# Kernel optimization log

Measured on AMD Instinct MI355X. Metric: run time of the kernel, lower is better.

## Reference

```python
import jax, jax.numpy as jnp
import numpy as np

EMBED, HEADS, LEVELS, POINTS = 256, 8, 4, 4
HD = EMBED // HEADS
BS, NQ = 2, 16384
SHAPES = [(128, 128), (64, 64), (32, 32), (16, 16)]  # (H, W) per level
NV = sum(h * w for h, w in SHAPES)
EPS = 1e-5


def layernorm(x, g, b):
    mu = jnp.mean(x, -1, keepdims=True)
    var = jnp.mean((x - mu) ** 2, -1, keepdims=True)
    return (x - mu) / jnp.sqrt(var + EPS) * g + b


def bilinear_sample(vl, loc, H, W):
    # vl: (bs, heads, H*W, hd); loc: (bs, nq, heads, P, 2) normalized [0,1]
    # grid_sample semantics: align_corners=False, zero padding
    x = loc[..., 0] * W - 0.5
    y = loc[..., 1] * H - 0.5
    x0 = jnp.floor(x)
    y0 = jnp.floor(y)
    lx, ly = x - x0, y - y0
    x0 = x0.astype(jnp.int32)
    y0 = y0.astype(jnp.int32)
    gather = jax.vmap(jax.vmap(lambda t, i: t[i]))  # over (bs, heads)
    acc = None
    for dx, dy, w in ((0, 0, (1 - lx) * (1 - ly)), (1, 0, lx * (1 - ly)),
                      (0, 1, (1 - lx) * ly), (1, 1, lx * ly)):
        xi, yi = x0 + dx, y0 + dy
        valid = ((xi >= 0) & (xi < W) & (yi >= 0) & (yi < H)).astype(vl.dtype)
        idx = jnp.clip(yi, 0, H - 1) * W + jnp.clip(xi, 0, W - 1)
        idx = idx.transpose(0, 2, 1, 3)           # (bs, heads, nq, P)
        g = gather(vl, idx)                       # (bs, heads, nq, P, hd)
        wv = (w * valid).transpose(0, 2, 1, 3)[..., None]
        acc = g * wv if acc is None else acc + g * wv
    return acc


def forward(lidar_feat, feat_flatten, ref_2d, spatial_shapes, level_start_index,
            q_pose, W_off, b_off, W_attn, b_attn, W_val, b_val, W_out, b_out,
            ln1_g, ln1_b, ffn_w1, ffn_w2, ln2_g, ln2_b):
    identity = lidar_feat                         # (nq, bs, C)
    q = (lidar_feat + q_pose).transpose(1, 0, 2)  # (bs, nq, C)
    bs, nq, C = q.shape
    v = feat_flatten.transpose(1, 0, 2) @ W_val + b_val
    v = v.reshape(bs, -1, HEADS, HD)
    off = (q @ W_off + b_off).reshape(bs, nq, HEADS, LEVELS, POINTS, 2)
    aw = (q @ W_attn + b_attn).reshape(bs, nq, HEADS, LEVELS * POINTS)
    aw = jax.nn.softmax(aw, -1).reshape(bs, nq, HEADS, LEVELS, POINTS)
    ss = np.asarray(spatial_shapes)               # static level shapes
    lsi = np.asarray(level_start_index)
    norm = jnp.asarray(ss[:, ::-1].copy(), q.dtype)  # (L, 2) [W, H]
    loc = ref_2d[:, :, None, :, None, :] + off / norm[None, None, None, :, None, :]
    out = jnp.zeros((bs, nq, HEADS, HD), q.dtype)
    for l in range(LEVELS):
        H, W = int(ss[l, 0]), int(ss[l, 1])
        s = int(lsi[l])
        vl = v[:, s:s + H * W].transpose(0, 2, 1, 3)   # (bs, heads, HW, hd)
        sampled = bilinear_sample(vl, loc[:, :, :, l], H, W)
        out = out + jnp.einsum('bhqpd,bqhp->bqhd', sampled, aw[:, :, :, l, :])
    out = out.reshape(bs, nq, C) @ W_out + b_out
    out = out.transpose(1, 0, 2) + identity       # residual (dropout=eval noop)
    x = layernorm(out, ln1_g, ln1_b)
    x = layernorm(jnp.maximum(x @ ffn_w1, 0.0) @ ffn_w2 + x, ln2_g, ln2_b)
    return x


def setup_inputs():
    key = jax.random.key(0)
    ks = jax.random.split(key, 16)
    starts = np.cumsum([0] + [h * w for h, w in SHAPES])[:-1]
    d = {
        'lidar_feat': jax.random.normal(ks[0], (NQ, BS, EMBED), jnp.float32),
        'feat_flatten': jax.random.normal(ks[1], (NV, BS, EMBED), jnp.float32),
        'ref_2d': jax.random.uniform(ks[2], (BS, NQ, LEVELS, 2), jnp.float32),
        'spatial_shapes': jnp.array(SHAPES, jnp.int32),
        'level_start_index': jnp.array(starts, jnp.int32),
        'q_pose': jax.random.normal(ks[3], (NQ, BS, EMBED), jnp.float32),
        'W_off': 0.02 * jax.random.normal(ks[4], (EMBED, HEADS * LEVELS * POINTS * 2), jnp.float32),
        'b_off': 2.0 * jax.random.normal(ks[5], (HEADS * LEVELS * POINTS * 2,), jnp.float32),
        'W_attn': 0.02 * jax.random.normal(ks[6], (EMBED, HEADS * LEVELS * POINTS), jnp.float32),
        'b_attn': jnp.zeros((HEADS * LEVELS * POINTS,), jnp.float32),
        'W_val': 0.02 * jax.random.normal(ks[7], (EMBED, EMBED), jnp.float32),
        'b_val': jnp.zeros((EMBED,), jnp.float32),
        'W_out': 0.02 * jax.random.normal(ks[8], (EMBED, EMBED), jnp.float32),
        'b_out': jnp.zeros((EMBED,), jnp.float32),
        'ln1_g': jnp.ones((EMBED,), jnp.float32),
        'ln1_b': jnp.zeros((EMBED,), jnp.float32),
        'ffn_w1': 0.02 * jax.random.normal(ks[9], (EMBED, EMBED), jnp.float32),
        'ffn_w2': 0.02 * jax.random.normal(ks[10], (EMBED, EMBED), jnp.float32),
        'ln2_g': jnp.ones((EMBED,), jnp.float32),
        'ln2_b': jnp.zeros((EMBED,), jnp.float32),
    }
    return d


def reference(lidar_feat, feat_flatten, ref_2d, spatial_shapes, level_start_index,
              q_pose, W_off, b_off, W_attn, b_attn, W_val, b_val, W_out, b_out,
              ln1_g, ln1_b, ffn_w1, ffn_w2, ln2_g, ln2_b):
    return forward(lidar_feat, feat_flatten, ref_2d, spatial_shapes,
                   level_start_index, q_pose, W_off, b_off, W_attn, b_attn,
                   W_val, b_val, W_out, b_out, ln1_g, ln1_b, ffn_w1, ffn_w2,
                   ln2_g, ln2_b)
```

## Files before the change

kernel.cpp:

```cpp
#include <hip/hip_runtime.h>
#include <cstdint>

#define EMBED 256
#define HEADS 8
#define LEVELS 4
#define POINTS 4
#define BS 2
#define NQ 16384
#define NV 21760
#define MQ (BS*NQ)
#define MV (BS*NV)
#define VAL_BLK 340
#define OA_BLK  256
#define BKT_BLK 64

typedef __attribute__((ext_vector_type(8))) short short8;
typedef __attribute__((ext_vector_type(4))) float f32x4;

__device__ __forceinline__ unsigned short f2bf(float f) {
    unsigned int u = __float_as_uint(f);
    u = (u + 0x7FFFu + ((u >> 16) & 1u)) >> 16;
    return (unsigned short)u;
}
__device__ __forceinline__ float bf2f(unsigned short h) {
    return __uint_as_float(((unsigned int)h) << 16);
}
__device__ __forceinline__ void glds16(const unsigned short* g, unsigned short* l) {
    __builtin_amdgcn_global_load_lds((const __attribute__((address_space(1))) void*)g,
                                     (__attribute__((address_space(3))) void*)l, 16, 0, 0);
}

struct WtArgs {
    const float* src[6];
    unsigned short* dst[6];
    int n[6];
};
__global__ __launch_bounds__(256) void prep_wt(WtArgs a, int* __restrict__ hist)
{
    const int t = threadIdx.x;
    if (blockIdx.x == 0 && blockIdx.y == 0) { hist[t] = 0; hist[t + 256] = 0; }
    const int g = blockIdx.y;
    const int N = a.n[g];
    const int e = blockIdx.x * 256 + t;
    if (e >= 256 * N) return;
    const int k = e / N, n = e - k * N;
    a.dst[g][(size_t)n * 256 + k] = f2bf(a.src[g][e]);
}

template<int NCOLS>
__device__ __forceinline__ void gemm_core(
    unsigned short* As, unsigned short* Bs, int bx,
    const float* __restrict__ Af, const float* __restrict__ A2f, int inner,
    const unsigned short* __restrict__ Bt,
    const float* __restrict__ bias0, const float* __restrict__ bias1,
    unsigned short* __restrict__ outh)
{
    constexpr int FN = NCOLS / 64;
    const int t = threadIdx.x, l = t & 63, w = t >> 6;
    const int wm = w >> 2, wn = w & 3;
    const int frow = l & 15, fgrp = l >> 4;
    const size_t brow = (size_t)bx * 128;

    const int fslot = fgrp ^ ((frow & 3) ^ ((frow >> 2) & 3));
    const int srow = l >> 2;
    const int sswz = (l & 3) ^ ((srow & 3) ^ ((srow >> 2) & 3));
    const unsigned short* gB0 = Bt + ((size_t)(w * 16 + srow)) * 256 + sswz * 8;

    const int arow_s = t >> 2, aslot_s = t & 3;
    const int grow = (int)brow + arow_s;
    const int bidx = grow / inner, nn = grow - bidx * inner;
    const float* srcA = Af + (size_t)(nn * BS + bidx) * 256;
    const float* srcA2 = A2f ? A2f + (size_t)(nn * BS + bidx) * 256 : nullptr;
    const int aswz_s = aslot_s ^ ((arow_s & 3) ^ ((arow_s >> 2) & 3));

    f32x4 acc[4][FN];
#pragma unroll
    for (int i = 0; i < 4; ++i)
#pragma unroll
        for (int j = 0; j < FN; ++j) acc[i][j] = f32x4{0.f, 0.f, 0.f, 0.f};

    float4 pA0 = *(const float4*)(srcA + aslot_s * 8);
    float4 pA1 = *(const float4*)(srcA + aslot_s * 8 + 4);
    float4 pC0, pC1;
    if (srcA2) { pC0 = *(const float4*)(srcA2 + aslot_s * 8);
                 pC1 = *(const float4*)(srcA2 + aslot_s * 8 + 4); }

    for (int k0 = 0; k0 < 256; k0 += 32) {
        glds16(gB0 + k0,         &Bs[w * 512]);
        glds16(gB0 + 32768 + k0, &Bs[(w + 8) * 512]);
        if constexpr (NCOLS == 384)
            glds16(gB0 + 65536 + k0, &Bs[(w + 16) * 512]);

        float c[8] = {pA0.x, pA0.y, pA0.z, pA0.w, pA1.x, pA1.y, pA1.z, pA1.w};
        if (srcA2) {
            c[0] += pC0.x; c[1] += pC0.y; c[2] += pC0.z; c[3] += pC0.w;
            c[4] += pC1.x; c[5] += pC1.y; c[6] += pC1.z; c[7] += pC1.w;
        }
        short8 pk;
#pragma unroll
        for (int i = 0; i < 8; ++i) pk[i] = (short)f2bf(c[i]);
        *reinterpret_cast<short8*>(&As[arow_s * 32 + aswz_s * 8]) = pk;
        if (k0 + 32 < 256) {
            pA0 = *(const float4*)(srcA + k0 + 32 + aslot_s * 8);
            pA1 = *(const float4*)(srcA + k0 + 32 + aslot_s * 8 + 4);
            if (srcA2) { pC0 = *(const float4*)(srcA2 + k0 + 32 + aslot_s * 8);
                         pC1 = *(const float4*)(srcA2 + k0 + 32 + aslot_s * 8 + 4); }
        }
        __syncthreads();

        short8 af[4]; short8 bq[FN];
#pragma unroll
        for (int fm = 0; fm < 4; ++fm)
            af[fm] = *reinterpret_cast<const short8*>(&As[(wm * 64 + fm * 16 + frow) * 32 + fslot * 8]);
#pragma unroll
        for (int fn = 0; fn < FN; ++fn)
            bq[fn] = *reinterpret_cast<const short8*>(&Bs[(wn * (NCOLS / 4) + fn * 16 + frow) * 32 + fslot * 8]);
#pragma unroll
        for (int fm = 0; fm < 4; ++fm)
#pragma unroll
            for (int fn = 0; fn < FN; ++fn)
                acc[fm][fn] = __builtin_amdgcn_mfma_f32_16x16x32_bf16(af[fm], bq[fn], acc[fm][fn], 0, 0, 0);
        __syncthreads();
    }

#pragma unroll
    for (int fn = 0; fn < FN; ++fn) {
        const int col = wn * (NCOLS / 4) + fn * 16 + frow;
        float b = 0.f;
        if (NCOLS == 384) b = (col < 256) ? bias0[col] : bias1[col - 256];
        else              b = bias0[col];
#pragma unroll
        for (int fm = 0; fm < 4; ++fm)
#pragma unroll
            for (int j = 0; j < 4; ++j) {
                const size_t row = brow + wm * 64 + fm * 16 + fgrp * 4 + j;
                outh[row * NCOLS + col] = f2bf(acc[fm][fn][j] + b);
            }
    }
}

__global__ __launch_bounds__(512) void valoa_k(
    const float* __restrict__ feat, const float* __restrict__ lidar,
    const float* __restrict__ q_pose, const float* __restrict__ ref2d,
    const unsigned short* __restrict__ wt_val, const unsigned short* __restrict__ wt_oa,
    const float* __restrict__ b_val, const float* __restrict__ b_off,
    const float* __restrict__ b_attn,
    unsigned short* __restrict__ vb, unsigned short* __restrict__ oa,
    int* __restrict__ bkt, int* __restrict__ hist)
{
    __shared__ unsigned short As[128 * 32];
    __shared__ unsigned short Bs[384 * 32];
    const int bx = blockIdx.x;
    if (bx < VAL_BLK) {
        gemm_core<256>(As, Bs, bx, feat, nullptr, NV, wt_val, b_val, nullptr, vb);
    } else if (bx < VAL_BLK + OA_BLK) {
        gemm_core<384>(As, Bs, bx - VAL_BLK, lidar, q_pose, NQ, wt_oa, b_off, b_attn, oa);
    } else {
        const int rb = (bx - VAL_BLK - OA_BLK) * 512 + threadIdx.x;
        const float x = ref2d[(size_t)rb * 8 + 0];
        const float y = ref2d[(size_t)rb * 8 + 1];
        const int qx = min(15, max(0, (int)(x * 16.f)));
        const int qy = min(15, max(0, (int)(y * 16.f)));
        const int bv = (rb >> 14) * 256 + qy * 16 + qx;
        bkt[rb] = bv;
        atomicAdd(&hist[bv], 1);
    }
}

__global__ __launch_bounds__(512) void scan_scatter_k(
    const int* __restrict__ hist, const int* __restrict__ bkt, int* __restrict__ perm)
{
    __shared__ int s[512];
    __shared__ int cur[512];
    const int t = threadIdx.x;
    const int v = hist[t];
    s[t] = v;
    __syncthreads();
    int acc = v;
#pragma unroll
    for (int o = 1; o < 512; o <<= 1) {
        const int add = (t >= o) ? s[t - o] : 0;
        __syncthreads();
        acc += add;
        s[t] = acc;
        __syncthreads();
    }
    cur[t] = acc - v;
    __syncthreads();
#pragma unroll 4
    for (int i = 0; i < 64; ++i) {
        const int rb = i * 512 + t;
        const int pos = atomicAdd(&cur[bkt[rb]], 1);
        perm[pos] = rb;
    }
}

__global__ __launch_bounds__(256) void sampler_k(
    const unsigned short* __restrict__ oa,
    const float* __restrict__ ref2d,
    const unsigned short* __restrict__ v,
    const int* __restrict__ perm,
    unsigned short* __restrict__ outh)
{
    const int bid = blockIdx.x;
    const int sbid = (bid & 7) * (MQ / 4 / 8) + (bid >> 3);
    const int q0 = sbid * 4;
    const int t = threadIdx.x;

    __shared__ uint2 s_d[4][8][4][17];

#pragma unroll
    for (int it = 0; it < 2; ++it) {
        const int item = t + it * 256;
        const int tq = item >> 7, hlp = item & 127;
        const int h = hlp >> 4, lp = hlp & 15, li = lp >> 2;
        const int rb = perm[q0 + tq];
        const int b = rb >> 14;

        const float2 refv = *(const float2*)(ref2d + (size_t)rb * 8 + li * 2);
        const ushort2 offu = *(const ushort2*)(oa + (size_t)rb * 384 + hlp * 2);
        const float ax = bf2f(oa[(size_t)rb * 384 + 256 + hlp]);

        float m = ax;
#pragma unroll
        for (int o = 1; o < 16; o <<= 1) m = fmaxf(m, __shfl_xor(m, o));
        const float e = __expf(ax - m);
        float sden = e;
#pragma unroll
        for (int o = 1; o < 16; o <<= 1) sden += __shfl_xor(sden, o);
        const float a = e / sden;

        const int Wl[4]  = {128, 64, 32, 16};
        const int S0l[4] = {0, 16384, 20480, 21504};
        const int Wi = Wl[li]; const float Wf = (float)Wi;
        const float x = (refv.x + bf2f(offu.x) / Wf) * Wf - 0.5f;
        const float y = (refv.y + bf2f(offu.y) / Wf) * Wf - 0.5f;
        const float x0f = floorf(x), y0f = floorf(y);
        const float lx = x - x0f, ly = y - y0f;
        const int x0 = (int)x0f, y0 = (int)y0f;
        const float cw[4] = {(1.f - lx) * (1.f - ly) * a, lx * (1.f - ly) * a,
                             (1.f - lx) * ly * a,          lx * ly * a};
        const int base = b * NV + S0l[li];
#pragma unroll
        for (int c = 0; c < 4; ++c) {
            const int xi = x0 + (c & 1), yi = y0 + (c >> 1);
            const bool val = (xi >= 0) & (xi < Wi) & (yi >= 0) & (yi < Wi);
            const int xc = min(max(xi, 0), Wi - 1), yc = min(max(yi, 0), Wi - 1);
            const unsigned int ofs = (unsigned int)(base + yc * Wi + xc) * 256u + h * 32;
            s_d[tq][h][c][lp] = make_uint2(__float_as_uint(val ? cw[c] : 0.f), ofs);
        }
    }
    __syncthreads();

    const int tq = t >> 6, l = t & 63, h = l >> 3, dq = l & 7;
    const int rb = perm[q0 + tq], b = rb >> 14, qi = rb & (NQ - 1);
    const unsigned short* vd = v + dq * 4;
    float a0 = 0.f, a1 = 0.f, a2 = 0.f, a3 = 0.f;
#pragma unroll
    for (int c = 0; c < 4; ++c) {
#pragma unroll
        for (int i = 0; i < 16; ++i) {
            const uint2 dd = s_d[tq][h][c][i];
            const uint2 raw = *(const uint2*)(vd + dd.y);
            const float wgt = __uint_as_float(dd.x);
            a0 += wgt * __uint_as_float(raw.x << 16);
            a1 += wgt * __uint_as_float(raw.x & 0xFFFF0000u);
            a2 += wgt * __uint_as_float(raw.y << 16);
            a3 += wgt * __uint_as_float(raw.y & 0xFFFF0000u);
        }
    }
    ushort4 o; o.x = f2bf(a0); o.y = f2bf(a1); o.z = f2bf(a2); o.w = f2bf(a3);
    *(ushort4*)(outh + (size_t)(qi * BS + b) * 256 + h * 32 + dq * 4) = o;
}

__global__ __launch_bounds__(512) void mega_k(
    const unsigned short* __restrict__ smp, const float* __restrict__ lidar,
    const unsigned short* __restrict__ Wo, const unsigned short* __restrict__ W1,
    const unsigned short* __restrict__ W2, const float* __restrict__ b_out,
    const float* __restrict__ ln1g, const float* __restrict__ ln1b,
    const float* __restrict__ ln2g, const float* __restrict__ ln2b,
    float* __restrict__ outf)
{
    __shared__ unsigned short XH[64 * 256];
    __shared__ unsigned short Bs[256 * 32];
    __shared__ float2 sdLN[64][4];

    const int t = threadIdx.x, l = t & 63, w = t >> 6;
    const int wm = w >> 2, wn = w & 3;
    const int frow = l & 15, fgrp = l >> 4;
    const size_t brow = (size_t)blockIdx.x * 64;

    const int fslot = fgrp ^ ((frow & 3) ^ ((frow >> 2) & 3));
    const int srow = l >> 2;
    const int sswz = (l & 3) ^ ((srow & 3) ^ ((srow >> 2) & 3));

    const unsigned short* gA  = smp + (brow + (size_t)((w & 3) * 16 + srow)) * 256 + sswz * 8;
    const unsigned short* gWo = Wo + ((size_t)(w * 16 + srow)) * 256 + sswz * 8;
    const unsigned short* gW1 = W1 + ((size_t)(w * 16 + srow)) * 256 + sswz * 8;
    const unsigned short* gW2 = W2 + ((size_t)(w * 16 + srow)) * 256 + sswz * 8;

    f32x4 acc[2][4];
    f32x4 xres[2][4];

#pragma unroll
    for (int i = 0; i < 2; ++i)
#pragma unroll
        for (int j = 0; j < 4; ++j) acc[i][j] = f32x4{0.f, 0.f, 0.f, 0.f};

    for (int k0 = 0; k0 < 256; k0 += 32) {
        glds16(gWo + k0,         &Bs[w * 512]);
        glds16(gWo + 32768 + k0, &Bs[(w + 8) * 512]);
        if (w < 4) glds16(gA + k0, &XH[w * 512]);
        __syncthreads();
        short8 af[2], bq[4];
#pragma unroll
        for (int fm = 0; fm < 2; ++fm)
            af[fm] = *reinterpret_cast<const short8*>(&XH[(wm * 32 + fm * 16 + frow) * 32 + fslot * 8]);
#pragma unroll
        for (int fn = 0; fn < 4; ++fn)
            bq[fn] = *reinterpret_cast<const short8*>(&Bs[(wn * 64 + fn * 16 + frow) * 32 + fslot * 8]);
#pragma unroll
        for (int fm = 0; fm < 2; ++fm)
#pragma unroll
            for (int fn = 0; fn < 4; ++fn)
                acc[fm][fn] = __builtin_amdgcn_mfma_f32_16x16x32_bf16(af[fm], bq[fn], acc[fm][fn], 0, 0, 0);
        __syncthreads();
    }

#pragma unroll
    for (int fm = 0; fm < 2; ++fm)
#pragma unroll
        for (int fn = 0; fn < 4; ++fn) {
            const int col = wn * 64 + fn * 16 + frow;
            const float bv = b_out[col];
#pragma unroll
            for (int j = 0; j < 4; ++j) {
                const size_t row = brow + wm * 32 + fm * 16 + fgrp * 4 + j;
                acc[fm][fn][j] += bv + lidar[row * 256 + col];
            }
        }
#pragma unroll
    for (int fm = 0; fm < 2; ++fm)
#pragma unroll
        for (int j = 0; j < 4; ++j) {
            float s1 = 0.f, s2 = 0.f;
#pragma unroll
            for (int fn = 0; fn < 4; ++fn) { const float x = acc[fm][fn][j]; s1 += x; s2 += x * x; }
#pragma unroll
            for (int o = 1; o < 16; o <<= 1) { s1 += __shfl_xor(s1, o); s2 += __shfl_xor(s2, o); }
            if (frow == 0) sdLN[wm * 32 + fm * 16 + fgrp * 4 + j][wn] = make_float2(s1, s2);
        }
    __syncthreads();
#pragma unroll
    for (int fm = 0; fm < 2; ++fm)
#pragma unroll
        for (int j = 0; j < 4; ++j) {
            const int rl = wm * 32 + fm * 16 + fgrp * 4 + j;
            const float2 p0 = sdLN[rl][0], p1 = sdLN[rl][1], p2 = sdLN[rl][2], p3 = sdLN[rl][3];
            const float s1 = p0.x + p1.x + p2.x + p3.x;
            const float s2 = p0.y + p1.y + p2.y + p3.y;
            const float mu = s1 * (1.f / 256.f);
            const float var = s2 * (1.f / 256.f) - mu * mu;
            const float rstd = rsqrtf(var + 1e-5f);
#pragma unroll
            for (int fn = 0; fn < 4; ++fn) {
                const int col = wn * 64 + fn * 16 + frow;
                const float y = (acc[fm][fn][j] - mu) * rstd * ln1g[col] + ln1b[col];
                xres[fm][fn][j] = y;
                const int ss = (col >> 3) ^ (rl & 7);
                XH[rl * 256 + ss * 8 + (col & 7)] = f2bf(y);
            }
        }
    __syncthreads();

#pragma unroll
    for (int i = 0; i < 2; ++i)
#pragma unroll
        for (int j = 0; j < 4; ++j) acc[i][j] = f32x4{0.f, 0.f, 0.f, 0.f};

    for (int k0 = 0; k0 < 256; k0 += 32) {
        glds16(gW1 + k0,         &Bs[w * 512]);
        glds16(gW1 + 32768 + k0, &Bs[(w + 8) * 512]);
        __syncthreads();
        short8 af[2], bq[4];
#pragma unroll
        for (int fm = 0; fm < 2; ++fm) {
            const int row = wm * 32 + fm * 16 + frow;
            const int ss = ((k0 >> 3) + fgrp) ^ (row & 7);
            af[fm] = *reinterpret_cast<const short8*>(&XH[row * 256 + ss * 8]);
        }
#pragma unroll
        for (int fn = 0; fn < 4; ++fn)
            bq[fn] = *reinterpret_cast<const short8*>(&Bs[(wn * 64 + fn * 16 + frow) * 32 + fslot * 8]);
#pragma unroll
        for (int fm = 0; fm < 2; ++fm)
#pragma unroll
            for (int fn = 0; fn < 4; ++fn)
                acc[fm][fn] = __builtin_amdgcn_mfma_f32_16x16x32_bf16(af[fm], bq[fn], acc[fm][fn], 0, 0, 0);
        __syncthreads();
    }

#pragma unroll
    for (int fm = 0; fm < 2; ++fm)
#pragma unroll
        for (int fn = 0; fn < 4; ++fn) {
            const int col = wn * 64 + fn * 16 + frow;
#pragma unroll
            for (int j = 0; j < 4; ++j) {
                const int rl = wm * 32 + fm * 16 + fgrp * 4 + j;
                const int ss = (col >> 3) ^ (rl & 7);
                XH[rl * 256 + ss * 8 + (col & 7)] = f2bf(fmaxf(acc[fm][fn][j], 0.f));
            }
        }
    __syncthreads();

#pragma unroll
    for (int i = 0; i < 2; ++i)
#pragma unroll
        for (int j = 0; j < 4; ++j) acc[i][j] = f32x4{0.f, 0.f, 0.f, 0.f};

    for (int k0 = 0; k0 < 256; k0 += 32) {
        glds16(gW2 + k0,         &Bs[w * 512]);
        glds16(gW2 + 32768 + k0, &Bs[(w + 8) * 512]);
        __syncthreads();
        short8 af[2], bq[4];
#pragma unroll
        for (int fm = 0; fm < 2; ++fm) {
            const int row = wm * 32 + fm * 16 + frow;
            const int ss = ((k0 >> 3) + fgrp) ^ (row & 7);
            af[fm] = *reinterpret_cast<const short8*>(&XH[row * 256 + ss * 8]);
        }
#pragma unroll
        for (int fn = 0; fn < 4; ++fn)
            bq[fn] = *reinterpret_cast<const short8*>(&Bs[(wn * 64 + fn * 16 + frow) * 32 + fslot * 8]);
#pragma unroll
        for (int fm = 0; fm < 2; ++fm)
#pragma unroll
            for (int fn = 0; fn < 4; ++fn)
                acc[fm][fn] = __builtin_amdgcn_mfma_f32_16x16x32_bf16(af[fm], bq[fn], acc[fm][fn], 0, 0, 0);
        __syncthreads();
    }

#pragma unroll
    for (int fm = 0; fm < 2; ++fm)
#pragma unroll
        for (int fn = 0; fn < 4; ++fn)
#pragma unroll
            for (int j = 0; j < 4; ++j) acc[fm][fn][j] += xres[fm][fn][j];
#pragma unroll
    for (int fm = 0; fm < 2; ++fm)
#pragma unroll
        for (int j = 0; j < 4; ++j) {
            float s1 = 0.f, s2 = 0.f;
#pragma unroll
            for (int fn = 0; fn < 4; ++fn) { const float x = acc[fm][fn][j]; s1 += x; s2 += x * x; }
#pragma unroll
            for (int o = 1; o < 16; o <<= 1) { s1 += __shfl_xor(s1, o); s2 += __shfl_xor(s2, o); }
            if (frow == 0) sdLN[wm * 32 + fm * 16 + fgrp * 4 + j][wn] = make_float2(s1, s2);
        }
    __syncthreads();
#pragma unroll
    for (int fm = 0; fm < 2; ++fm)
#pragma unroll
        for (int j = 0; j < 4; ++j) {
            const int rl = wm * 32 + fm * 16 + fgrp * 4 + j;
            const float2 p0 = sdLN[rl][0], p1 = sdLN[rl][1], p2 = sdLN[rl][2], p3 = sdLN[rl][3];
            const float s1 = p0.x + p1.x + p2.x + p3.x;
            const float s2 = p0.y + p1.y + p2.y + p3.y;
            const float mu = s1 * (1.f / 256.f);
            const float var = s2 * (1.f / 256.f) - mu * mu;
            const float rstd = rsqrtf(var + 1e-5f);
            const size_t row = brow + rl;
#pragma unroll
            for (int fn = 0; fn < 4; ++fn) {
                const int col = wn * 64 + fn * 16 + frow;
                outf[row * 256 + col] = (acc[fm][fn][j] - mu) * rstd * ln2g[col] + ln2b[col];
            }
        }
}

extern "C" void kernel_launch(void* const* d_in, const int* in_sizes, int n_in,
                              void* d_out, int out_size, void* d_ws, size_t ws_size,
                              hipStream_t stream)
{
    const float* lidar  = (const float*)d_in[0];
    const float* feat   = (const float*)d_in[1];
    const float* ref2d  = (const float*)d_in[2];
    const float* q_pose = (const float*)d_in[5];
    const float* W_off  = (const float*)d_in[6];
    const float* b_off  = (const float*)d_in[7];
    const float* W_attn = (const float*)d_in[8];
    const float* b_attn = (const float*)d_in[9];
    const float* W_val  = (const float*)d_in[10];
    const float* b_val  = (const float*)d_in[11];
    const float* W_out  = (const float*)d_in[12];
    const float* b_out  = (const float*)d_in[13];
    const float* ln1_g  = (const float*)d_in[14];
    const float* ln1_b  = (const float*)d_in[15];
    const float* ffn_w1 = (const float*)d_in[16];
    const float* ffn_w2 = (const float*)d_in[17];
    const float* ln2_g  = (const float*)d_in[18];
    const float* ln2_b  = (const float*)d_in[19];

    float* out = (float*)d_out;
    char*  ws  = (char*)d_ws;

    unsigned short* vb   = (unsigned short*)(ws + 0);
    unsigned short* oa   = (unsigned short*)(ws + 22282240);
    unsigned short* smp  = (unsigned short*)(ws + 47448064);
    unsigned short* wt   = (unsigned short*)(ws + 64225280);
    int* perm = (int*)(ws + 64946176);
    int* bkt  = (int*)(ws + 65077248);
    int* hist = (int*)(ws + 65208320);
    unsigned short* wt_val = wt;
    unsigned short* wt_oa  = wt + 65536;
    unsigned short* wt_out = wt + 163840;
    unsigned short* wt_f1  = wt + 229376;
    unsigned short* wt_f2  = wt + 294912;

    WtArgs wa;
    wa.src[0] = W_val;  wa.dst[0] = wt_val;          wa.n[0] = 256;
    wa.src[1] = W_off;  wa.dst[1] = wt_oa;           wa.n[1] = 256;
    wa.src[2] = W_attn; wa.dst[2] = wt_oa + 65536;   wa.n[2] = 128;
    wa.src[3] = W_out;  wa.dst[3] = wt_out;          wa.n[3] = 256;
    wa.src[4] = ffn_w1; wa.dst[4] = wt_f1;           wa.n[4] = 256;
    wa.src[5] = ffn_w2; wa.dst[5] = wt_f2;           wa.n[5] = 256;

    prep_wt<<<dim3(384, 6), dim3(256), 0, stream>>>(wa, hist);

    valoa_k<<<dim3(VAL_BLK + OA_BLK + BKT_BLK), dim3(512), 0, stream>>>(
        feat, lidar, q_pose, ref2d, wt_val, wt_oa, b_val, b_off, b_attn,
        vb, oa, bkt, hist);

    scan_scatter_k<<<dim3(1), dim3(512), 0, stream>>>(hist, bkt, perm);

    sampler_k<<<dim3(MQ / 4), dim3(256), 0, stream>>>(oa, ref2d, vb, perm, smp);

    mega_k<<<dim3(MQ / 64), dim3(512), 0, stream>>>(
        smp, lidar, wt_out, wt_f1, wt_f2, b_out,
        ln1_g, ln1_b, ln2_g, ln2_b, out);
}
```

Before: 212.2 us.

## Store value projection in fp32 and fold bucketing and scan into earlier kernels

The value projection output changes from bf16 to fp32, so the sampler gathers float4 per corner and no longer unpacks bf16. Query bucketing moves into the weight-prep kernel as an extra grid row, and the histogram is now zeroed with a memset. The prefix scan and scatter now run in one extra block of the GEMM kernel, which removes a separate launch. The cost is twice the value buffer footprint and twice the gather traffic in the sampler, since each 16-byte load now holds four floats instead of eight halves.

```diff
diff --git a/kernel.cpp b/kernel.cpp
--- a/kernel.cpp
+++ b/kernel.cpp
@@ -12,7 +12,6 @@
 #define MV (BS*NV)
 #define VAL_BLK 340
 #define OA_BLK  256
-#define BKT_BLK 64
 
 typedef __attribute__((ext_vector_type(8))) short short8;
 typedef __attribute__((ext_vector_type(4))) float f32x4;
@@ -35,13 +34,29 @@
     unsigned short* dst[6];
     int n[6];
 };
-__global__ __launch_bounds__(256) void prep_wt(WtArgs a, int* __restrict__ hist)
+__global__ __launch_bounds__(256) void prep_wt(
+    WtArgs a, const float* __restrict__ ref2d,
+    int* __restrict__ bkt, int* __restrict__ hist)
 {
-    const int t = threadIdx.x;
-    if (blockIdx.x == 0 && blockIdx.y == 0) { hist[t] = 0; hist[t + 256] = 0; }
-    const int g = blockIdx.y;
+    const int t = threadIdx.x, g = blockIdx.y, bx = blockIdx.x;
+    if (g == 6) {
+        if (bx < 64) {
+#pragma unroll
+            for (int i = 0; i < 2; ++i) {
+                const int rb = bx * 512 + i * 256 + t;
+                const float x = ref2d[(size_t)rb * 8 + 0];
+                const float y = ref2d[(size_t)rb * 8 + 1];
+                const int qx = min(15, max(0, (int)(x * 16.f)));
+                const int qy = min(15, max(0, (int)(y * 16.f)));
+                const int bv = (rb >> 14) * 256 + qy * 16 + qx;
+                bkt[rb] = bv;
+                atomicAdd(&hist[bv], 1);
+            }
+        }
+        return;
+    }
     const int N = a.n[g];
-    const int e = blockIdx.x * 256 + t;
+    const int e = bx * 256 + t;
     if (e >= 256 * N) return;
     const int k = e / N, n = e - k * N;
     a.dst[g][(size_t)n * 256 + k] = f2bf(a.src[g][e]);
@@ -53,7 +68,7 @@
     const float* __restrict__ Af, const float* __restrict__ A2f, int inner,
     const unsigned short* __restrict__ Bt,
     const float* __restrict__ bias0, const float* __restrict__ bias1,
-    unsigned short* __restrict__ outh)
+    float* __restrict__ outf, unsigned short* __restrict__ outh)
 {
     constexpr int FN = NCOLS / 64;
     const int t = threadIdx.x, l = t & 63, w = t >> 6;
@@ -134,71 +149,61 @@
 #pragma unroll
             for (int j = 0; j < 4; ++j) {
                 const size_t row = brow + wm * 64 + fm * 16 + fgrp * 4 + j;
-                outh[row * NCOLS + col] = f2bf(acc[fm][fn][j] + b);
+                const float x = acc[fm][fn][j] + b;
+                if (outf) outf[row * NCOLS + col] = x;
+                else      outh[row * NCOLS + col] = f2bf(x);
             }
     }
 }
 
 __global__ __launch_bounds__(512) void valoa_k(
     const float* __restrict__ feat, const float* __restrict__ lidar,
-    const float* __restrict__ q_pose, const float* __restrict__ ref2d,
+    const float* __restrict__ q_pose,
     const unsigned short* __restrict__ wt_val, const unsigned short* __restrict__ wt_oa,
     const float* __restrict__ b_val, const float* __restrict__ b_off,
     const float* __restrict__ b_attn,
-    unsigned short* __restrict__ vb, unsigned short* __restrict__ oa,
-    int* __restrict__ bkt, int* __restrict__ hist)
+    float* __restrict__ vb, unsigned short* __restrict__ oa,
+    const int* __restrict__ hist, const int* __restrict__ bkt,
+    int* __restrict__ perm)
 {
     __shared__ unsigned short As[128 * 32];
     __shared__ unsigned short Bs[384 * 32];
     const int bx = blockIdx.x;
     if (bx < VAL_BLK) {
-        gemm_core<256>(As, Bs, bx, feat, nullptr, NV, wt_val, b_val, nullptr, vb);
+        gemm_core<256>(As, Bs, bx, feat, nullptr, NV, wt_val, b_val, nullptr, vb, nullptr);
     } else if (bx < VAL_BLK + OA_BLK) {
-        gemm_core<384>(As, Bs, bx - VAL_BLK, lidar, q_pose, NQ, wt_oa, b_off, b_attn, oa);
+        gemm_core<384>(As, Bs, bx - VAL_BLK, lidar, q_pose, NQ, wt_oa, b_off, b_attn, nullptr, oa);
     } else {
-        const int rb = (bx - VAL_BLK - OA_BLK) * 512 + threadIdx.x;
-        const float x = ref2d[(size_t)rb * 8 + 0];
-        const float y = ref2d[(size_t)rb * 8 + 1];
-        const int qx = min(15, max(0, (int)(x * 16.f)));
-        const int qy = min(15, max(0, (int)(y * 16.f)));
-        const int bv = (rb >> 14) * 256 + qy * 16 + qx;
-        bkt[rb] = bv;
-        atomicAdd(&hist[bv], 1);
-    }
-}
-
-__global__ __launch_bounds__(512) void scan_scatter_k(
-    const int* __restrict__ hist, const int* __restrict__ bkt, int* __restrict__ perm)
-{
-    __shared__ int s[512];
-    __shared__ int cur[512];
-    const int t = threadIdx.x;
-    const int v = hist[t];
-    s[t] = v;
-    __syncthreads();
-    int acc = v;
-#pragma unroll
-    for (int o = 1; o < 512; o <<= 1) {
-        const int add = (t >= o) ? s[t - o] : 0;
-        __syncthreads();
-        acc += add;
-        s[t] = acc;
-        __syncthreads();
-    }
-    cur[t] = acc - v;
-    __syncthreads();
+        int* s   = (int*)As;
+        int* cur = ((int*)As) + 512;
+        const int t = threadIdx.x;
+        const int v = hist[t];
+        s[t] = v;
+        __syncthreads();
+        int acc = v;
+#pragma unroll
+        for (int o = 1; o < 512; o <<= 1) {
+            const int add = (t >= o) ? s[t - o] : 0;
+            __syncthreads();
+            acc += add;
+            s[t] = acc;
+            __syncthreads();
+        }
+        cur[t] = acc - v;
+        __syncthreads();
 #pragma unroll 4
-    for (int i = 0; i < 64; ++i) {
-        const int rb = i * 512 + t;
-        const int pos = atomicAdd(&cur[bkt[rb]], 1);
-        perm[pos] = rb;
+        for (int i = 0; i < 64; ++i) {
+            const int rb = i * 512 + t;
+            const int pos = atomicAdd(&cur[bkt[rb]], 1);
+            perm[pos] = rb;
+        }
     }
 }
 
 __global__ __launch_bounds__(256) void sampler_k(
     const unsigned short* __restrict__ oa,
     const float* __restrict__ ref2d,
-    const unsigned short* __restrict__ v,
+    const float* __restrict__ v,
     const int* __restrict__ perm,
     unsigned short* __restrict__ outh)
 {
@@ -246,7 +251,7 @@
             const int xi = x0 + (c & 1), yi = y0 + (c >> 1);
             const bool val = (xi >= 0) & (xi < Wi) & (yi >= 0) & (yi < Wi);
             const int xc = min(max(xi, 0), Wi - 1), yc = min(max(yi, 0), Wi - 1);
-            const unsigned int ofs = (unsigned int)(base + yc * Wi + xc) * 256u + h * 32;
+            const unsigned int ofs = (unsigned int)(base + yc * Wi + xc) * 1024u + h * 128u;
             s_d[tq][h][c][lp] = make_uint2(__float_as_uint(val ? cw[c] : 0.f), ofs);
         }
     }
@@ -254,19 +259,19 @@
 
     const int tq = t >> 6, l = t & 63, h = l >> 3, dq = l & 7;
     const int rb = perm[q0 + tq], b = rb >> 14, qi = rb & (NQ - 1);
-    const unsigned short* vd = v + dq * 4;
+    const char* vq = (const char*)v + dq * 16u;
     float a0 = 0.f, a1 = 0.f, a2 = 0.f, a3 = 0.f;
 #pragma unroll
     for (int c = 0; c < 4; ++c) {
 #pragma unroll
         for (int i = 0; i < 16; ++i) {
             const uint2 dd = s_d[tq][h][c][i];
-            const uint2 raw = *(const uint2*)(vd + dd.y);
+            const float4 raw = *(const float4*)(vq + dd.y);
             const float wgt = __uint_as_float(dd.x);
-            a0 += wgt * __uint_as_float(raw.x << 16);
-            a1 += wgt * __uint_as_float(raw.x & 0xFFFF0000u);
-            a2 += wgt * __uint_as_float(raw.y << 16);
-            a3 += wgt * __uint_as_float(raw.y & 0xFFFF0000u);
+            a0 += wgt * raw.x;
+            a1 += wgt * raw.y;
+            a2 += wgt * raw.z;
+            a3 += wgt * raw.w;
         }
     }
     ushort4 o; o.x = f2bf(a0); o.y = f2bf(a1); o.z = f2bf(a2); o.w = f2bf(a3);
@@ -505,13 +510,13 @@
     float* out = (float*)d_out;
     char*  ws  = (char*)d_ws;
 
-    unsigned short* vb   = (unsigned short*)(ws + 0);
-    unsigned short* oa   = (unsigned short*)(ws + 22282240);
-    unsigned short* smp  = (unsigned short*)(ws + 47448064);
-    unsigned short* wt   = (unsigned short*)(ws + 64225280);
-    int* perm = (int*)(ws + 64946176);
-    int* bkt  = (int*)(ws + 65077248);
-    int* hist = (int*)(ws + 65208320);
+    float*          vb   = (float*)(ws + 0);
+    unsigned short* oa   = (unsigned short*)(ws + 44564480);
+    unsigned short* smp  = (unsigned short*)(ws + 69730304);
+    unsigned short* wt   = (unsigned short*)(ws + 86507520);
+    int* perm = (int*)(ws + 87228416);
+    int* bkt  = (int*)(ws + 87359488);
+    int* hist = (int*)(ws + 87490560);
     unsigned short* wt_val = wt;
     unsigned short* wt_oa  = wt + 65536;
     unsigned short* wt_out = wt + 163840;
@@ -526,13 +531,13 @@
     wa.src[4] = ffn_w1; wa.dst[4] = wt_f1;           wa.n[4] = 256;
     wa.src[5] = ffn_w2; wa.dst[5] = wt_f2;           wa.n[5] = 256;
 
-    prep_wt<<<dim3(384, 6), dim3(256), 0, stream>>>(wa, hist);
-
-    valoa_k<<<dim3(VAL_BLK + OA_BLK + BKT_BLK), dim3(512), 0, stream>>>(
-        feat, lidar, q_pose, ref2d, wt_val, wt_oa, b_val, b_off, b_attn,
-        vb, oa, bkt, hist);
-
-    scan_scatter_k<<<dim3(1), dim3(512), 0, stream>>>(hist, bkt, perm);
+    hipMemsetAsync(hist, 0, 2048, stream);
+
+    prep_wt<<<dim3(384, 7), dim3(256), 0, stream>>>(wa, ref2d, bkt, hist);
+
+    valoa_k<<<dim3(VAL_BLK + OA_BLK + 1), dim3(512), 0, stream>>>(
+        feat, lidar, q_pose, wt_val, wt_oa, b_val, b_off, b_attn,
+        vb, oa, hist, bkt, perm);
 
     sampler_k<<<dim3(MQ / 4), dim3(256), 0, stream>>>(oa, ref2d, vb, perm, smp);
 
```

New measurement: 220.4 us. 1.04x slower.
